# Performance work log

Hardware: AMD Instinct MI355X
Metric: run time of the kernel (lower is better)

The kernel has to match this reference:

```python
import jax, jax.numpy as jnp
import numpy as np

N = 50000          # nodes
E = 800000         # edges (avg degree 16)
C = 64             # hidden_channels
MC = 128           # message_channels = 2*C
EDGE_IN = 3 * C + 4
UPD_IN = C + MC + C


def _mlp(x, w1, b1, w2, b2, w3, b3):
    h1 = jax.nn.gelu(x @ w1 + b1, approximate=False)  # torch nn.GELU default = exact erf
    h2 = jax.nn.gelu(h1 @ w2 + b2, approximate=False)
    return h2 @ w3 + b3


def _layernorm(x, g, b, eps=1e-5):
    mu = x.mean(-1, keepdims=True)
    var = ((x - mu) ** 2).mean(-1, keepdims=True)
    return (x - mu) * jax.lax.rsqrt(var + eps) * g + b


def _forward(edge_index, coords, h, flow_dir, ln_g, ln_b,
             ew1, eb1, ew2, eb2, ew3, eb3,
             gw1, gb1, gw2, gb2,
             glw1, glb1, glw2, glb2, glw3, glb3,
             uw1, ub1, uw2, ub2, uw3, ub3, res_scale):
    x = coords[0]                       # [N,3]
    feat = _layernorm(h[0], ln_g, ln_b) # [N,C]
    u = flow_dir[0]
    u = u / (jnp.linalg.norm(u) + 1e-8)
    row, col = edge_index[0], edge_index[1]
    xi, xj = x[row], x[col]             # [E,3] gathers
    rel = xi - xj
    dist2 = (rel * rel).sum(-1, keepdims=True)
    xi_dot_u = (xi * u).sum(-1, keepdims=True)
    xj_dot_u = (xj * u).sum(-1, keepdims=True)
    rel_dot_u = (rel * u).sum(-1, keepdims=True)
    fi, fj = feat[row], feat[col]       # [E,C]
    fd = fi - fj
    edge_input = jnp.concatenate([fi, fj, fd, dist2, xi_dot_u, xj_dot_u, rel_dot_u], axis=-1)  # [E, 3C+4]
    edge_hidden = _mlp(edge_input, ew1, eb1, ew2, eb2, ew3, eb3)  # [E, MC]
    gate = jax.nn.sigmoid(jax.nn.gelu(edge_hidden @ gw1 + gb1, approximate=False) @ gw2 + gb2)  # [E,1]
    msg = gate * edge_hidden
    agg = jax.ops.segment_sum(msg, row, num_segments=N)                       # [N, MC]
    deg = jax.ops.segment_sum(jnp.ones((E, 1), feat.dtype), row, num_segments=N)
    agg = agg / jnp.maximum(deg, 1.0)
    global_feat = feat.mean(0, keepdims=True)                                  # [1,C]
    global_ctx = _mlp(global_feat, glw1, glb1, glw2, glb2, glw3, glb3)        # [1,C]
    global_node = jnp.broadcast_to(global_ctx, (feat.shape[0], global_ctx.shape[-1]))
    update_input = jnp.concatenate([feat, agg, global_node], axis=-1)          # [N, C+MC+C]
    dh = _mlp(update_input, uw1, ub1, uw2, ub2, uw3, ub3)                      # [N,C]
    return (jnp.tanh(res_scale) * dh)[None]                                    # [1,N,C]


def setup_inputs() -> dict:
    key = jax.random.key(0)
    ks = iter(jax.random.split(key, 40))
    def nrm(shape, scale=0.05):
        return (jax.random.normal(next(ks), shape, jnp.float32) * scale)
    return {
        "coords": jax.random.normal(next(ks), (1, N, 3), jnp.float32),
        "h": jax.random.normal(next(ks), (1, N, C), jnp.float32),
        "flow_dir": jax.random.normal(next(ks), (1, 3), jnp.float32),
        "edge_index": jax.random.randint(next(ks), (2, E), 0, N, dtype=jnp.int32),
        "ln_g": jnp.ones((C,), jnp.float32), "ln_b": jnp.zeros((C,), jnp.float32),
        "ew1": nrm((EDGE_IN, MC)), "eb1": jnp.zeros((MC,), jnp.float32),
        "ew2": nrm((MC, MC)), "eb2": jnp.zeros((MC,), jnp.float32),
        "ew3": nrm((MC, MC)), "eb3": jnp.zeros((MC,), jnp.float32),
        "gw1": nrm((MC, MC)), "gb1": jnp.zeros((MC,), jnp.float32),
        "gw2": nrm((MC, 1)), "gb2": jnp.zeros((1,), jnp.float32),
        "glw1": nrm((C, C)), "glb1": jnp.zeros((C,), jnp.float32),
        "glw2": nrm((C, C)), "glb2": jnp.zeros((C,), jnp.float32),
        "glw3": nrm((C, C)), "glb3": jnp.zeros((C,), jnp.float32),
        "uw1": nrm((UPD_IN, MC)), "ub1": jnp.zeros((MC,), jnp.float32),
        "uw2": nrm((MC, MC)), "ub2": jnp.zeros((MC,), jnp.float32),
        "uw3": nrm((MC, C)), "ub3": jnp.zeros((C,), jnp.float32),
        "res_scale": jnp.float32(0.15),
    }


def reference(coords, h, flow_dir, edge_index, ln_g, ln_b,
              ew1, eb1, ew2, eb2, ew3, eb3,
              gw1, gb1, gw2, gb2,
              glw1, glb1, glw2, glb2, glw3, glb3,
              uw1, ub1, uw2, ub2, uw3, ub3, res_scale):
    return _forward(edge_index, coords, h, flow_dir, ln_g, ln_b,
                    ew1, eb1, ew2, eb2, ew3, eb3,
                    gw1, gb1, gw2, gb2,
                    glw1, glb1, glw2, glb2, glw3, glb3,
                    uw1, ub1, uw2, ub2, uw3, ub3, res_scale)
```

## Files before the change

kernel.cpp:

```cpp
#include <hip/hip_runtime.h>
#include <hip/hip_bf16.h>
#include <math.h>

#define N_NODES 50000
#define N_EDGES 800000
#define CDIM 64
#define MCDIM 128
#define GSUM_REP 32

#define XS1 168
#define HS  136
#define UST 264

typedef __attribute__((ext_vector_type(8))) short short8;
typedef __attribute__((ext_vector_type(4))) float floatx4;
typedef __attribute__((ext_vector_type(2))) float f32x2;

__device__ __forceinline__ float gelu_fast(float x) {
    float z = fabsf(x) * 0.70710678f;
    float w = fmaf(z, fmaf(z, fmaf(z, fmaf(z, 0.078108f, 0.000972f),
                                   0.230389f), 0.278393f), 1.0f);
    float w2 = w * w;
    float r = __builtin_amdgcn_rcpf(w2 * w2);
    float m = 0.5f * fabsf(x);
    return fmaf(-m, r, fmaf(0.5f, x, m));
}

__device__ __forceinline__ f32x2 gelu_pk(f32x2 x) {
    f32x2 ax = __builtin_elementwise_abs(x);
    f32x2 z = ax * 0.70710678f;
    f32x2 w = z * (z * (z * (z * 0.078108f + 0.000972f) + 0.230389f)
                   + 0.278393f) + 1.0f;
    f32x2 w2 = w * w;
    f32x2 w4 = w2 * w2;
    f32x2 r;
    r.x = __builtin_amdgcn_rcpf(w4.x);
    r.y = __builtin_amdgcn_rcpf(w4.y);
    f32x2 m = 0.5f * ax;
    return 0.5f * x + m - m * r;
}

__device__ __forceinline__ unsigned short f2bf(float f) {
    unsigned int u = __float_as_uint(f);
    unsigned int r = u + 0x7fffu + ((u >> 16) & 1u);
    return (unsigned short)(r >> 16);
}
__device__ __forceinline__ float bf2f(unsigned int lo16) {
    return __uint_as_float(lo16 << 16);
}
__device__ __forceinline__ unsigned int f2bf2(float lo, float hi) {
    __hip_bfloat162 v = __float22bfloat162_rn(make_float2(lo, hi));
    union { __hip_bfloat162 b; unsigned int u; } cv;
    cv.b = v;
    return cv.u;
}
__device__ __forceinline__ ushort4 pack4(float4 v) {
    ushort4 r;
    r.x = f2bf(v.x); r.y = f2bf(v.y); r.z = f2bf(v.z); r.w = f2bf(v.w);
    return r;
}

#define F1_OFF 0
#define F2_OFF (5 * 4096)
#define F3_OFF (9 * 4096)
#define FG_OFF (13 * 4096)
#define FU1_OFF (17 * 4096)
#define FU2_OFF (25 * 4096)
#define FU3_OFF (29 * 4096)
#define FRAG_TOTAL (29 * 4096 + 4 * 2048)

__global__ __launch_bounds__(256) void prep_frags(
    const float* __restrict__ ew1, const float* __restrict__ ew2,
    const float* __restrict__ ew3, const float* __restrict__ gw1,
    const float* __restrict__ uw1, const float* __restrict__ uw2,
    const float* __restrict__ uw3, unsigned short* __restrict__ frags,
    int* __restrict__ deg_int, float* __restrict__ gsum) {
    int idx = blockIdx.x * 256 + threadIdx.x;
    if (idx < N_NODES) deg_int[idx] = 0;
    if (idx < GSUM_REP * 64) gsum[idx] = 0.0f;
    if (idx >= FRAG_TOTAL) return;
    if (idx < F2_OFF) {
        int chunk = idx >> 12;
        int rem = idx & 4095;
        int ct = rem >> 9;
        int lane = (rem >> 3) & 63;
        int j = rem & 7;
        int k = chunk * 32 + (lane >> 4) * 8 + j;
        int n = ct * 16 + (lane & 15);
        float v;
        if (k < 64)       v = ew1[k * 128 + n] + ew1[(128 + k) * 128 + n];
        else if (k < 128) v = ew1[k * 128 + n] - ew1[(64 + k) * 128 + n];
        else if (k < 132) v = ew1[(192 + k - 128) * 128 + n];
        else              v = 0.0f;
        frags[idx] = f2bf(v);
    } else if (idx < FU3_OFF) {
        int chunk = idx >> 12;
        int rem = idx & 4095;
        int ct = rem >> 9;
        int lane = (rem >> 3) & 63;
        int j = rem & 7;
        const float* W; int kbase;
        if (chunk < 9)       { W = ew2; kbase = (chunk - 5) * 32; }
        else if (chunk < 13) { W = ew3; kbase = (chunk - 9) * 32; }
        else if (chunk < 17) { W = gw1; kbase = (chunk - 13) * 32; }
        else if (chunk < 25) { W = uw1; kbase = (chunk - 17) * 32; }
        else                 { W = uw2; kbase = (chunk - 25) * 32; }
        int k = kbase + (lane >> 4) * 8 + j;
        int n = ct * 16 + (lane & 15);
        frags[idx] = f2bf(W[k * 128 + n]);
    } else {
        int rem = idx - FU3_OFF;
        int chunk = rem >> 11;
        int r = rem & 2047;
        int ct = r >> 9;
        int lane = (r >> 3) & 63;
        int j = r & 7;
        int k = chunk * 32 + (lane >> 4) * 8 + j;
        int n = ct * 16 + (lane & 15);
        frags[idx] = f2bf(uw3[k * 64 + n]);
    }
}

template <int NCT>
__device__ __forceinline__ void bias_init(floatx4* acc,
                                          const float* __restrict__ bias, int lane) {
    int c = lane & 15;
#pragma unroll
    for (int ct = 0; ct < NCT; ct++) {
        float b = bias[ct * 16 + c];
        acc[ct][0] = b; acc[ct][1] = b; acc[ct][2] = b; acc[ct][3] = b;
    }
}

template <int NCH, int NCT>
__device__ __forceinline__ void mfma_layer(const unsigned short* Xl, int xs,
                                           const unsigned short* __restrict__ F,
                                           int lane, floatx4* acc) {
    int q = lane >> 4, c = lane & 15;
    const unsigned short* xrow = Xl + c * xs + q * 8;
    for (int k0 = 0; k0 < NCH; k0++) {
        short8 a = *(const short8*)(xrow + k0 * 32);
#pragma unroll
        for (int ct = 0; ct < NCT; ct++) {
            short8 b = *(const short8*)(F + ((k0 * NCT + ct) * 64 + lane) * 8);
            acc[ct] = __builtin_amdgcn_mfma_f32_16x16x32_bf16(a, b, acc[ct], 0, 0, 0);
        }
    }
}

template <bool GELU, int NCT>
__device__ __forceinline__ void epilogue_store(floatx4* acc,
                                               unsigned short* dst, int xs, int lane) {
    int q = lane >> 4, c = lane & 15;
    unsigned short* base = dst + (q * 4) * xs + c;
#pragma unroll
    for (int ct = 0; ct < NCT; ct++) {
        f32x2 v01 = {acc[ct][0], acc[ct][1]};
        f32x2 v23 = {acc[ct][2], acc[ct][3]};
        if (GELU) { v01 = gelu_pk(v01); v23 = gelu_pk(v23); }
        unsigned int p01 = f2bf2(v01.x, v01.y), p23 = f2bf2(v23.x, v23.y);
        unsigned short* p = base + ct * 16;
        p[0]      = (unsigned short)p01;
        p[xs]     = (unsigned short)(p01 >> 16);
        p[2 * xs] = (unsigned short)p23;
        p[3 * xs] = (unsigned short)(p23 >> 16);
    }
}

__global__ __launch_bounds__(256) void ln_count_kernel(
    const float* __restrict__ h, const float* __restrict__ ln_g,
    const float* __restrict__ ln_b, const float* __restrict__ flow_dir,
    const int* __restrict__ eidx, unsigned short* __restrict__ featb,
    float* __restrict__ gsum, float* __restrict__ u_out,
    int* __restrict__ deg_int) {
    int t = threadIdx.x;
    int ln = t >> 6;
    int c = t & 63;
    int n = blockIdx.x * 4 + ln;

    float x = h[n * CDIM + c];
    float s = x;
#pragma unroll
    for (int off = 32; off > 0; off >>= 1) s += __shfl_xor(s, off, 64);
    float mu = s * (1.0f / 64.0f);
    float d = x - mu;
    float v = d * d;
#pragma unroll
    for (int off = 32; off > 0; off >>= 1) v += __shfl_xor(v, off, 64);
    float rs = 1.0f / sqrtf(v * (1.0f / 64.0f) + 1e-5f);
    float f = d * rs * ln_g[c] + ln_b[c];
    featb[n * CDIM + c] = f2bf(f);

    __shared__ float fs[4][64];
    fs[ln][c] = f;
    __syncthreads();
    if (t < 64) {
        float p = fs[0][t] + fs[1][t] + fs[2][t] + fs[3][t];
        atomicAdd(&gsum[(blockIdx.x & (GSUM_REP - 1)) * 64 + t], p);
        int e = blockIdx.x * 64 + t;
        atomicAdd(&deg_int[eidx[e]], 1);
    }
    if (blockIdx.x == 0 && t == 0) {
        float ux = flow_dir[0], uy = flow_dir[1], uz = flow_dir[2];
        float nrm = sqrtf(ux * ux + uy * uy + uz * uz) + 1e-8f;
        u_out[0] = ux / nrm;
        u_out[1] = uy / nrm;
        u_out[2] = uz / nrm;
    }
}

__global__ __launch_bounds__(1024) void mid_kernel(
    const int* __restrict__ deg_int, int* __restrict__ rowstart,
    int* __restrict__ cursor,
    const float* __restrict__ gsum,
    const float* __restrict__ glw1, const float* __restrict__ glb1,
    const float* __restrict__ glw2, const float* __restrict__ glb2,
    const float* __restrict__ glw3, const float* __restrict__ glb3,
    const float* __restrict__ res_scale,
    unsigned short* __restrict__ gctxb, float* __restrict__ tres) {
    int t = threadIdx.x;
    if (blockIdx.x == 0) {
        __shared__ int wsum[16];
        __shared__ int run;
        int wid = t >> 6, lane = t & 63;
        int4 vs[13];
#pragma unroll
        for (int chunk = 0; chunk < 13; chunk++) {
            int base = chunk * 4096 + t * 4;
            int4 v = {0, 0, 0, 0};
            if (base + 3 < N_NODES) {
                v = *(const int4*)(deg_int + base);
            } else {
                if (base < N_NODES) v.x = deg_int[base];
                if (base + 1 < N_NODES) v.y = deg_int[base + 1];
                if (base + 2 < N_NODES) v.z = deg_int[base + 2];
                if (base + 3 < N_NODES) v.w = deg_int[base + 3];
            }
            vs[chunk] = v;
        }
        if (t == 0) run = 0;
        __syncthreads();
#pragma unroll
        for (int chunk = 0; chunk < 13; chunk++) {
            int base = chunk * 4096 + t * 4;
            int4 v = vs[chunk];
            int s1 = v.x, s2 = s1 + v.y, s3 = s2 + v.z, s4 = s3 + v.w;
            int x = s4;
#pragma unroll
            for (int off = 1; off < 64; off <<= 1) {
                int y = __shfl_up(x, off, 64);
                if (lane >= off) x += y;
            }
            if (lane == 63) wsum[wid] = x;
            __syncthreads();
            if (t < 16) {
                int sv = wsum[t];
#pragma unroll
                for (int off = 1; off < 16; off <<= 1) {
                    int y = __shfl_up(sv, off, 16);
                    if (t >= off) sv += y;
                }
                wsum[t] = sv;
            }
            __syncthreads();
            int run_l = run;
            int wpre = (wid == 0) ? 0 : wsum[wid - 1];
            int toff = run_l + wpre + (x - s4);
            int e0 = toff, e1 = toff + s1, e2 = toff + s2, e3 = toff + s3;
            if (base <= N_NODES) rowstart[base] = e0;
            if (base + 1 <= N_NODES) rowstart[base + 1] = e1;
            if (base + 2 <= N_NODES) rowstart[base + 2] = e2;
            if (base + 3 <= N_NODES) rowstart[base + 3] = e3;
            if (base < N_NODES) cursor[base] = e0;
            if (base + 1 < N_NODES) cursor[base + 1] = e1;
            if (base + 2 < N_NODES) cursor[base + 2] = e2;
            if (base + 3 < N_NODES) cursor[base + 3] = e3;
            __syncthreads();
            if (t == 0) run = run_l + wsum[15];
            __syncthreads();
        }
    } else {
        __shared__ float a[64], b[64];
        float s = 0.0f;
        if (t < 64) {
            float acc = 0.0f;
            for (int r = 0; r < GSUM_REP; r++) acc += gsum[r * 64 + t];
            a[t] = acc * (1.0f / (float)N_NODES);
        }
        __syncthreads();
        if (t < 64) {
            s = glb1[t];
            for (int k = 0; k < 64; k++) s += a[k] * glw1[k * 64 + t];
            b[t] = gelu_fast(s);
        }
        __syncthreads();
        if (t < 64) {
            s = glb2[t];
            for (int k = 0; k < 64; k++) s += b[k] * glw2[k * 64 + t];
        }
        __syncthreads();
        if (t < 64) a[t] = gelu_fast(s);
        __syncthreads();
        if (t < 64) {
            s = glb3[t];
            for (int k = 0; k < 64; k++) s += a[k] * glw3[k * 64 + t];
            gctxb[t] = f2bf(s);
        }
        if (t == 0) *tres = tanhf(res_scale[0]);
    }
}

struct SmemE {
    unsigned short x1[64 * XS1];
    float gate[64];
    int pos[64];
    int rows[64];
};

__global__ __launch_bounds__(256, 5) void edge_kernel(
    const float* __restrict__ coords, const int* __restrict__ eidx,
    const unsigned short* __restrict__ featb, const float* __restrict__ u,
    const unsigned short* __restrict__ frags,
    const float* __restrict__ eb1, const float* __restrict__ eb2,
    const float* __restrict__ eb3,
    const float* __restrict__ gb1, const float* __restrict__ gw2,
    const float* __restrict__ gb2,
    int* __restrict__ cursor, unsigned short* __restrict__ msg,
    float* __restrict__ agg, int use_msg) {
    __shared__ SmemE sm;
    int t = threadIdx.x;
    int wv = t >> 6;
    int lane = t & 63;
    int e0 = blockIdx.x * 64;
    unsigned short* slice = sm.x1 + wv * 16 * XS1;

    {
        int le = t >> 2, sub = t & 3;
        int e = e0 + le;
        int row = eidx[e];
        int col = eidx[N_EDGES + e];
        const uint4* fi4 = (const uint4*)(featb + (long)row * CDIM);
        const uint4* fj4 = (const uint4*)(featb + (long)col * CDIM);
        unsigned short* xr = sm.x1 + le * XS1;
        *(uint4*)(xr + sub * 16) = fi4[sub * 2];
        *(uint4*)(xr + sub * 16 + 8) = fi4[sub * 2 + 1];
        *(uint4*)(xr + 64 + sub * 16) = fj4[sub * 2];
        *(uint4*)(xr + 64 + sub * 16 + 8) = fj4[sub * 2 + 1];
        ushort4 z = {0, 0, 0, 0};
        if (sub == 0) {
            sm.rows[le] = row;
            sm.pos[le] = atomicAdd(&cursor[row], 1);
            float xix = coords[row * 3], xiy = coords[row * 3 + 1], xiz = coords[row * 3 + 2];
            float xjx = coords[col * 3], xjy = coords[col * 3 + 1], xjz = coords[col * 3 + 2];
            float rx = xix - xjx, ry = xiy - xjy, rz = xiz - xjz;
            float ux = u[0], uy = u[1], uz = u[2];
            float4 sc;
            sc.x = rx * rx + ry * ry + rz * rz;
            sc.y = xix * ux + xiy * uy + xiz * uz;
            sc.z = xjx * ux + xjy * uy + xjz * uz;
            sc.w = rx * ux + ry * uy + rz * uz;
            *(ushort4*)(xr + 128) = pack4(sc);
        } else if (sub == 1) {
            *(ushort4*)(xr + 132) = z; *(ushort4*)(xr + 136) = z; *(ushort4*)(xr + 140) = z;
        } else if (sub == 2) {
            *(ushort4*)(xr + 144) = z; *(ushort4*)(xr + 148) = z;
        } else {
            *(ushort4*)(xr + 152) = z; *(ushort4*)(xr + 156) = z;
        }
    }
    __syncthreads();

    floatx4 acc[8];

    bias_init<8>(acc, eb1, lane);
    mfma_layer<5, 8>(slice, XS1, frags + F1_OFF, lane, acc);
    epilogue_store<true, 8>(acc, slice, HS, lane);
    __syncthreads();

    bias_init<8>(acc, eb2, lane);
    mfma_layer<4, 8>(slice, HS, frags + F2_OFF, lane, acc);
    epilogue_store<true, 8>(acc, slice, HS, lane);
    __syncthreads();

    floatx4 h3[8];
    bias_init<8>(h3, eb3, lane);
    mfma_layer<4, 8>(slice, HS, frags + F3_OFF, lane, h3);
    epilogue_store<false, 8>(h3, slice, HS, lane);
    __syncthreads();

    bias_init<8>(acc, gb1, lane);
    mfma_layer<4, 8>(slice, HS, frags + FG_OFF, lane, acc);
    {
        int q = lane >> 4, c = lane & 15;
        f32x2 p01 = {0.0f, 0.0f}, p23 = {0.0f, 0.0f};
#pragma unroll
        for (int ct = 0; ct < 8; ct++) {
            float w2 = gw2[ct * 16 + c];
            f32x2 g01 = gelu_pk((f32x2){acc[ct][0], acc[ct][1]});
            f32x2 g23 = gelu_pk((f32x2){acc[ct][2], acc[ct][3]});
            p01 += g01 * w2;
            p23 += g23 * w2;
        }
        float p[4] = {p01.x, p01.y, p23.x, p23.y};
#pragma unroll
        for (int i = 0; i < 4; i++) {
#pragma unroll
            for (int mask = 1; mask < 16; mask <<= 1) p[i] += __shfl_xor(p[i], mask, 64);
        }
        if (c == 0) {
            float gb = gb2[0];
#pragma unroll
            for (int i = 0; i < 4; i++) {
                float z = p[i] + gb;
                sm.gate[wv * 16 + q * 4 + i] = 1.0f / (1.0f + __expf(-z));
            }
        }
    }
    __syncthreads();

    if (use_msg) {
        {
            int q = lane >> 4, c = lane & 15;
            unsigned short* base = slice + (q * 4) * HS + c;
            float gv[4];
#pragma unroll
            for (int i = 0; i < 4; i++) gv[i] = sm.gate[wv * 16 + q * 4 + i];
#pragma unroll
            for (int ct = 0; ct < 8; ct++) {
                unsigned int p01 = f2bf2(h3[ct][0] * gv[0], h3[ct][1] * gv[1]);
                unsigned int p23 = f2bf2(h3[ct][2] * gv[2], h3[ct][3] * gv[3]);
                unsigned short* p = base + ct * 16;
                p[0] = (unsigned short)p01;
                p[HS] = (unsigned short)(p01 >> 16);
                p[2 * HS] = (unsigned short)p23;
                p[3 * HS] = (unsigned short)(p23 >> 16);
            }
        }
        __syncthreads();
        {
            int le = t >> 2, sub = t & 3;
            long base = (long)sm.pos[le] * MCDIM;
            const unsigned short* src = sm.x1 + (le >> 4) * 16 * XS1 + (le & 15) * HS;
#pragma unroll
            for (int m = 0; m < 4; m++) {
                int off = m * 32 + sub * 8;
                *(short8*)(msg + base + off) = *(const short8*)(src + off);
            }
        }
    } else {
        int q = lane >> 4, c = lane & 15;
#pragma unroll
        for (int i = 0; i < 4; i++) {
            int e = wv * 16 + q * 4 + i;
            int row = sm.rows[e];
            float g = sm.gate[e];
            float* agr = agg + (long)row * MCDIM;
#pragma unroll
            for (int ct = 0; ct < 8; ct++)
                atomicAdd(agr + ct * 16 + c, g * h3[ct][i]);
        }
    }
}

__global__ __launch_bounds__(256) void gather_kernel(
    const int* __restrict__ rowstart, const unsigned short* __restrict__ msg,
    const float* __restrict__ agg, int use_msg,
    unsigned short* __restrict__ aggb) {
    int wv = threadIdx.x >> 6, lane = threadIdx.x & 63;
    int n = blockIdx.x * 4 + wv;
    if (n >= N_NODES) return;
    int rs = rowstart[n], re = rowstart[n + 1];
    int deg = re - rs;
    float a0 = 0.0f, a1 = 0.0f, a2 = 0.0f, a3 = 0.0f;
    if (use_msg) {
        const unsigned short* base = msg + (long)rs * MCDIM;
        int pairs = deg >> 1;
        for (int i = 0; i < pairs; i++) {
            uint2 v = *(const uint2*)(base + i * 256 + lane * 4);
            a0 += bf2f(v.x & 0xffffu); a1 += bf2f(v.x >> 16);
            a2 += bf2f(v.y & 0xffffu); a3 += bf2f(v.y >> 16);
        }
        if ((deg & 1) && lane < 32) {
            uint2 v = *(const uint2*)(base + (deg - 1) * MCDIM + lane * 4);
            a0 += bf2f(v.x & 0xffffu); a1 += bf2f(v.x >> 16);
            a2 += bf2f(v.y & 0xffffu); a3 += bf2f(v.y >> 16);
        }
        a0 += __shfl_xor(a0, 32, 64);
        a1 += __shfl_xor(a1, 32, 64);
        a2 += __shfl_xor(a2, 32, 64);
        a3 += __shfl_xor(a3, 32, 64);
    } else if (lane < 32) {
        const float4 v = *(const float4*)(agg + (long)n * MCDIM + lane * 4);
        a0 = v.x; a1 = v.y; a2 = v.z; a3 = v.w;
    }
    if (lane < 32) {
        float inv = 1.0f / fmaxf((float)deg, 1.0f);
        uint2 o;
        o.x = f2bf2(a0 * inv, a1 * inv);
        o.y = f2bf2(a2 * inv, a3 * inv);
        *(uint2*)(aggb + (long)n * MCDIM + lane * 4) = o;
    }
}

struct SmemU {
    unsigned short ui[64 * UST];
};

__global__ __launch_bounds__(256, 4) void update_kernel(
    const unsigned short* __restrict__ featb, const unsigned short* __restrict__ aggb,
    const unsigned short* __restrict__ gctxb, const float* __restrict__ tres,
    const unsigned short* __restrict__ frags,
    const float* __restrict__ ub1, const float* __restrict__ ub2,
    const float* __restrict__ ub3,
    float* __restrict__ out) {
    __shared__ SmemU sm;
    int t = threadIdx.x;
    int wv = t >> 6;
    int lane = t & 63;
    int n0 = blockIdx.x * 64;
    unsigned short* slice = sm.ui + wv * 16 * UST;

    {
        int ln = t >> 2, sub = t & 3;
        int n = n0 + ln;
        unsigned short* ur = sm.ui + ln * UST;
        if (n < N_NODES) {
            const uint4* f4 = (const uint4*)(featb + (long)n * CDIM);
            *(uint4*)(ur + sub * 16) = f4[sub * 2];
            *(uint4*)(ur + sub * 16 + 8) = f4[sub * 2 + 1];
            const uint4* a4 = (const uint4*)(aggb + (long)n * MCDIM);
            *(uint4*)(ur + 64 + sub * 32) = a4[sub * 4];
            *(uint4*)(ur + 64 + sub * 32 + 8) = a4[sub * 4 + 1];
            *(uint4*)(ur + 64 + sub * 32 + 16) = a4[sub * 4 + 2];
            *(uint4*)(ur + 64 + sub * 32 + 24) = a4[sub * 4 + 3];
            const uint4* g4 = (const uint4*)gctxb;
            *(uint4*)(ur + 192 + sub * 16) = g4[sub * 2];
            *(uint4*)(ur + 192 + sub * 16 + 8) = g4[sub * 2 + 1];
        } else {
            uint4 z = {0, 0, 0, 0};
#pragma unroll
            for (int m = 0; m < 8; m++) *(uint4*)(ur + sub * 64 + m * 8) = z;
        }
    }
    __syncthreads();

    floatx4 acc[8];
    bias_init<8>(acc, ub1, lane);
    mfma_layer<8, 8>(slice, UST, frags + FU1_OFF, lane, acc);
    epilogue_store<true, 8>(acc, slice, HS, lane);
    __syncthreads();

    bias_init<8>(acc, ub2, lane);
    mfma_layer<4, 8>(slice, HS, frags + FU2_OFF, lane, acc);
    epilogue_store<true, 8>(acc, slice, HS, lane);
    __syncthreads();

    floatx4 acc3[4];
    bias_init<4>(acc3, ub3, lane);
    mfma_layer<4, 4>(slice, HS, frags + FU3_OFF, lane, acc3);
    {
        int q = lane >> 4, c = lane & 15;
        float tr = *tres;
#pragma unroll
        for (int ct = 0; ct < 4; ct++) {
#pragma unroll
            for (int i = 0; i < 4; i++) {
                int n = n0 + wv * 16 + q * 4 + i;
                if (n < N_NODES) out[(long)n * CDIM + ct * 16 + c] = acc3[ct][i] * tr;
            }
        }
    }
}

extern "C" void kernel_launch(void* const* d_in, const int* in_sizes, int n_in,
                              void* d_out, int out_size, void* d_ws, size_t ws_size,
                              hipStream_t stream) {
    const float* coords = (const float*)d_in[0];
    const float* h = (const float*)d_in[1];
    const float* flow = (const float*)d_in[2];
    const int* eidx = (const int*)d_in[3];
    const float* ln_g = (const float*)d_in[4];
    const float* ln_b = (const float*)d_in[5];
    const float* ew1 = (const float*)d_in[6];
    const float* eb1 = (const float*)d_in[7];
    const float* ew2 = (const float*)d_in[8];
    const float* eb2 = (const float*)d_in[9];
    const float* ew3 = (const float*)d_in[10];
    const float* eb3 = (const float*)d_in[11];
    const float* gw1 = (const float*)d_in[12];
    const float* gb1 = (const float*)d_in[13];
    const float* gw2 = (const float*)d_in[14];
    const float* gb2 = (const float*)d_in[15];
    const float* glw1 = (const float*)d_in[16];
    const float* glb1 = (const float*)d_in[17];
    const float* glw2 = (const float*)d_in[18];
    const float* glb2 = (const float*)d_in[19];
    const float* glw3 = (const float*)d_in[20];
    const float* glb3 = (const float*)d_in[21];
    const float* uw1 = (const float*)d_in[22];
    const float* ub1 = (const float*)d_in[23];
    const float* uw2 = (const float*)d_in[24];
    const float* ub2 = (const float*)d_in[25];
    const float* uw3 = (const float*)d_in[26];
    const float* ub3 = (const float*)d_in[27];
    const float* res = (const float*)d_in[28];

    char* base = (char*)d_ws;
    unsigned short* frags = (unsigned short*)base;
    unsigned short* featb = (unsigned short*)(base + FRAG_TOTAL * 2);
    unsigned short* aggb = featb + (size_t)N_NODES * CDIM;
    unsigned short* gctxb = aggb + (size_t)N_NODES * MCDIM;
    float* gsum = (float*)(gctxb + 64);
    float* u = gsum + GSUM_REP * 64;
    float* tres = u + 4;
    int* rowstart = (int*)(tres + 1);
    int* cursor = rowstart + (N_NODES + 1);
    int* deg_int = cursor + N_NODES;
    char* tail = (char*)(deg_int + N_NODES);
    tail = (char*)(((uintptr_t)tail + 255) & ~(uintptr_t)255);
    size_t head_bytes = (size_t)(tail - base);
    size_t msg_bytes = (size_t)N_EDGES * MCDIM * 2;
    int use_msg = (ws_size >= head_bytes + msg_bytes) ? 1 : 0;
    unsigned short* msg = (unsigned short*)tail;
    float* agg = (float*)tail;

    if (!use_msg)
        hipMemsetAsync(agg, 0, (size_t)N_NODES * MCDIM * sizeof(float), stream);

    prep_frags<<<FRAG_TOTAL / 256, 256, 0, stream>>>(ew1, ew2, ew3, gw1,
                                                     uw1, uw2, uw3, frags,
                                                     deg_int, gsum);
    ln_count_kernel<<<N_NODES / 4, 256, 0, stream>>>(h, ln_g, ln_b, flow, eidx,
                                                     featb, gsum, u, deg_int);
    mid_kernel<<<2, 1024, 0, stream>>>(deg_int, rowstart, cursor, gsum,
                                       glw1, glb1, glw2, glb2, glw3, glb3,
                                       res, gctxb, tres);
    edge_kernel<<<N_EDGES / 64, 256, 0, stream>>>(coords, eidx, featb, u, frags,
                                                  eb1, eb2, eb3, gb1, gw2, gb2,
                                                  cursor, msg, agg, use_msg);
    gather_kernel<<<(N_NODES + 3) / 4, 256, 0, stream>>>(rowstart, msg, agg,
                                                         use_msg, aggb);
    update_kernel<<<(N_NODES + 63) / 64, 256, 0, stream>>>(featb, aggb, gctxb,
                                                           tres, frags,
                                                           ub1, ub2, ub3,
                                                           (float*)d_out);
}
```

Before: 529.9 us.

## Fold ew3 into gate first layer so gate and layer 3 run in parallel

The edge MLP's third linear layer (no activation) is composed with the gate's first linear layer on the host-side prep kernel: W' = ew3·gw1 and b' = gb1 + eb3·gw1. The gate now reads the layer-2 activations directly, and layer 3 is computed afterwards from the same slice, removing one epilogue store to shared memory and one block barrier in the edge kernel. Gate MFMA work stays the same size. The fused weights are rounded to bf16 after an fp32 product, which slightly changes numerics. The prep kernel gains a 128-term dot product per gate fragment element.

```diff
diff --git a/kernel.cpp b/kernel.cpp
--- a/kernel.cpp
+++ b/kernel.cpp
@@ -72,12 +72,19 @@
 __global__ __launch_bounds__(256) void prep_frags(
     const float* __restrict__ ew1, const float* __restrict__ ew2,
     const float* __restrict__ ew3, const float* __restrict__ gw1,
+    const float* __restrict__ eb3, const float* __restrict__ gb1,
     const float* __restrict__ uw1, const float* __restrict__ uw2,
     const float* __restrict__ uw3, unsigned short* __restrict__ frags,
-    int* __restrict__ deg_int, float* __restrict__ gsum) {
+    int* __restrict__ deg_int, float* __restrict__ gsum,
+    float* __restrict__ egb) {
     int idx = blockIdx.x * 256 + threadIdx.x;
     if (idx < N_NODES) deg_int[idx] = 0;
     if (idx < GSUM_REP * 64) gsum[idx] = 0.0f;
+    if (idx < 128) {
+        float s = gb1[idx];
+        for (int jj = 0; jj < 128; jj++) s += eb3[jj] * gw1[jj * 128 + idx];
+        egb[idx] = s;
+    }
     if (idx >= FRAG_TOTAL) return;
     if (idx < F2_OFF) {
         int chunk = idx >> 12;
@@ -93,6 +100,17 @@
         else if (k < 132) v = ew1[(192 + k - 128) * 128 + n];
         else              v = 0.0f;
         frags[idx] = f2bf(v);
+    } else if (idx >= FG_OFF && idx < FU1_OFF) {
+        int chunk = idx >> 12;
+        int rem = idx & 4095;
+        int ct = rem >> 9;
+        int lane = (rem >> 3) & 63;
+        int j = rem & 7;
+        int k = (chunk - 13) * 32 + (lane >> 4) * 8 + j;
+        int n = ct * 16 + (lane & 15);
+        float s = 0.0f;
+        for (int jj = 0; jj < 128; jj++) s += ew3[k * 128 + jj] * gw1[jj * 128 + n];
+        frags[idx] = f2bf(s);
     } else if (idx < FU3_OFF) {
         int chunk = idx >> 12;
         int rem = idx & 4095;
@@ -102,7 +120,6 @@
         const float* W; int kbase;
         if (chunk < 9)       { W = ew2; kbase = (chunk - 5) * 32; }
         else if (chunk < 13) { W = ew3; kbase = (chunk - 9) * 32; }
-        else if (chunk < 17) { W = gw1; kbase = (chunk - 13) * 32; }
         else if (chunk < 25) { W = uw1; kbase = (chunk - 17) * 32; }
         else                 { W = uw2; kbase = (chunk - 25) * 32; }
         int k = kbase + (lane >> 4) * 8 + j;
@@ -323,7 +340,7 @@
     const unsigned short* __restrict__ frags,
     const float* __restrict__ eb1, const float* __restrict__ eb2,
     const float* __restrict__ eb3,
-    const float* __restrict__ gb1, const float* __restrict__ gw2,
+    const float* __restrict__ egb, const float* __restrict__ gw2,
     const float* __restrict__ gb2,
     int* __restrict__ cursor, unsigned short* __restrict__ msg,
     float* __restrict__ agg, int use_msg) {
@@ -382,13 +399,7 @@
     epilogue_store<true, 8>(acc, slice, HS, lane);
     __syncthreads();
 
-    floatx4 h3[8];
-    bias_init<8>(h3, eb3, lane);
-    mfma_layer<4, 8>(slice, HS, frags + F3_OFF, lane, h3);
-    epilogue_store<false, 8>(h3, slice, HS, lane);
-    __syncthreads();
-
-    bias_init<8>(acc, gb1, lane);
+    bias_init<8>(acc, egb, lane);
     mfma_layer<4, 8>(slice, HS, frags + FG_OFF, lane, acc);
     {
         int q = lane >> 4, c = lane & 15;
@@ -416,7 +427,10 @@
             }
         }
     }
-    __syncthreads();
+
+    floatx4 h3[8];
+    bias_init<8>(h3, eb3, lane);
+    mfma_layer<4, 8>(slice, HS, frags + F3_OFF, lane, h3);
 
     if (use_msg) {
         {
@@ -613,7 +627,8 @@
     float* gsum = (float*)(gctxb + 64);
     float* u = gsum + GSUM_REP * 64;
     float* tres = u + 4;
-    int* rowstart = (int*)(tres + 1);
+    float* egb = tres + 1;
+    int* rowstart = (int*)(egb + 128);
     int* cursor = rowstart + (N_NODES + 1);
     int* deg_int = cursor + N_NODES;
     char* tail = (char*)(deg_int + N_NODES);
@@ -628,15 +643,16 @@
         hipMemsetAsync(agg, 0, (size_t)N_NODES * MCDIM * sizeof(float), stream);
 
     prep_frags<<<FRAG_TOTAL / 256, 256, 0, stream>>>(ew1, ew2, ew3, gw1,
+                                                     eb3, gb1,
                                                      uw1, uw2, uw3, frags,
-                                                     deg_int, gsum);
+                                                     deg_int, gsum, egb);
     ln_count_kernel<<<N_NODES / 4, 256, 0, stream>>>(h, ln_g, ln_b, flow, eidx,
                                                      featb, gsum, u, deg_int);
     mid_kernel<<<2, 1024, 0, stream>>>(deg_int, rowstart, cursor, gsum,
                                        glw1, glb1, glw2, glb2, glw3, glb3,
                                        res, gctxb, tres);
     edge_kernel<<<N_EDGES / 64, 256, 0, stream>>>(coords, eidx, featb, u, frags,
-                                                  eb1, eb2, eb3, gb1, gw2, gb2,
+                                                  eb1, eb2, eb3, egb, gw2, gb2,
                                                   cursor, msg, agg, use_msg);
     gather_kernel<<<(N_NODES + 3) / 4, 256, 0, stream>>>(rowstart, msg, agg,
                                                          use_msg, aggb);
```

Result: faster. 503.9 us (-4.9%).
